# Kernel optimization log

Measured on AMD Instinct MI355X. Metric: run time of the kernel, lower is better.

## Reference

```python
import jax, jax.numpy as jnp
import numpy as np

HIDDEN = 1024
HEADS = 16
BATCH = 2
SEQ = 2048
# dropout_p = 0.1 but module evaluated in eval mode (training=False) -> identity


def setup_inputs() -> dict:
    key = jax.random.key(0)
    k1, k2, k3 = jax.random.split(key, 3)
    x = jax.random.normal(k1, (BATCH, SEQ, HIDDEN), dtype=jnp.float32)
    # unit-scaling Linear: weight ~ N(0,1) (reset_parameters uses nn.init.normal_)
    w_qkv = jax.random.normal(k2, (3 * HIDDEN, HIDDEN), dtype=jnp.float32)
    w_o = jax.random.normal(k3, (HIDDEN, HIDDEN), dtype=jnp.float32)
    return {"x": x, "w_qkv": w_qkv, "w_o": w_o}


def reference(x, w_qkv, w_o):
    b, s, hid = x.shape
    heads = HEADS
    d = hid // heads
    # unit-scaled linear (constraint='to_output_scale'): y = x @ W.T * fan_in**-0.5
    qkv = (x @ w_qkv.T) * (hid ** -0.5)            # [b, s, 3*hid]
    # einops 'b s (z h d) -> z b h s d'
    qkv = qkv.reshape(b, s, 3, heads, d)
    q = jnp.transpose(qkv[:, :, 0], (0, 2, 1, 3))   # [b, h, s, d]
    k = jnp.transpose(qkv[:, :, 1], (0, 2, 1, 3))
    v = jnp.transpose(qkv[:, :, 2], (0, 2, 1, 3))
    # unit-scaled matmul: scale = inner_dim**-0.5
    scores = jnp.einsum('bhqd,bhkd->bhqk', q, k) * (d ** -0.5)  # [b, h, s, s]
    # unit-scaled softmax: output_scale = n / sqrt(n - 1)
    attn = jax.nn.softmax(scores, axis=-1) * (s / np.sqrt(s - 1.0))
    # dropout inactive (eval mode)
    out = jnp.einsum('bhqk,bhkd->bhqd', attn, v) * (s ** -0.5)  # inner dim = s
    out = jnp.transpose(out, (0, 2, 1, 3)).reshape(b, s, hid)   # 'b h s d -> b s (h d)'
    return (out @ w_o.T) * (hid ** -0.5)
```

## Files before the change

### kernel.cpp

```cpp
#include <hip/hip_runtime.h>

typedef unsigned short u16;
typedef _Float16 f16x8 __attribute__((ext_vector_type(8)));
typedef float f32x4 __attribute__((ext_vector_type(4)));
typedef unsigned short u16x4 __attribute__((ext_vector_type(4)));

#define HID 1024
#define SEQ 2048
#define NH 16
#define DH 64

__device__ __forceinline__ u16 f2h(float f) {
  return __builtin_bit_cast(u16, (_Float16)f);
}
__device__ __forceinline__ f32x4 mfma_h(f16x8 a, f16x8 b, f32x4 c) {
  return __builtin_amdgcn_mfma_f32_16x16x32_f16(a, b, c, 0, 0, 0);
}
__device__ __forceinline__ float fexp2(float x) {
#if __has_builtin(__builtin_amdgcn_exp2f)
  return __builtin_amdgcn_exp2f(x);
#else
  return __expf(0.69314718f * x);
#endif
}
__device__ __forceinline__ void g2l16(const u16* g, u16* l) {
  __builtin_amdgcn_global_load_lds(
      (const __attribute__((address_space(1))) unsigned int*)g,
      (__attribute__((address_space(3))) unsigned int*)l, 16, 0, 0);
}

#define NX4 ((4096 * 1024) / 4)
#define NQ4 ((3072 * 1024) / 4)
#define NO4 ((1024 * 1024) / 4)
__global__ __launch_bounds__(256) void prep_kernel(
    const float* __restrict__ x, const float* __restrict__ wq,
    const float* __restrict__ wo,
    u16* __restrict__ x16, u16* __restrict__ wq16, u16* __restrict__ wo16) {
  int i = blockIdx.x * 256 + threadIdx.x;
  const float4 v = (i < NX4) ? ((const float4*)x)[i]
                 : (i < NX4 + NQ4) ? ((const float4*)wq)[i - NX4]
                 : ((const float4*)wo)[i - NX4 - NQ4];
  u16* dst = (i < NX4) ? &x16[(size_t)i * 4]
           : (i < NX4 + NQ4) ? &wq16[(size_t)(i - NX4) * 4]
           : &wo16[(size_t)(i - NX4 - NQ4) * 4];
  u16x4 o;
  o[0] = f2h(v.x); o[1] = f2h(v.y); o[2] = f2h(v.z); o[3] = f2h(v.w);
  *(u16x4*)dst = o;
}

__global__ __launch_bounds__(256, 3) void gemm_qkv(
    const u16* __restrict__ a16, const u16* __restrict__ b16,
    u16* __restrict__ qf, u16* __restrict__ kf, u16* __restrict__ vtf) {
  __shared__ __align__(16) u16 la[128 * 32], lb[128 * 32];
  const int t = threadIdx.x;
  const int lane = t & 63, w = t >> 6;
  const int wr = w >> 1, wc = w & 1;
  const int lr = lane & 15, lg = lane >> 4;
  const int br = blockIdx.x, bc = blockIdx.y;
  const f32x4 fzero = {0.f, 0.f, 0.f, 0.f};
  f32x4 acc[4][4];
#pragma unroll
  for (int i = 0; i < 4; ++i)
#pragma unroll
    for (int j = 0; j < 4; ++j) acc[i][j] = fzero;
  const int srow = t >> 2, scol = (t & 3) << 3;
  const u16* ga = a16 + (size_t)(br * 128 + srow) * HID + scol;
  const u16* gb = b16 + (size_t)(bc * 128 + srow) * HID + scol;
  const int lo16 = t * 8;
  for (int kk = 0; kk < HID; kk += 32) {
    g2l16(ga + kk, &la[lo16]);
    g2l16(ga + kk + (size_t)64 * HID, &la[lo16 + 2048]);
    g2l16(gb + kk, &lb[lo16]);
    g2l16(gb + kk + (size_t)64 * HID, &lb[lo16 + 2048]);
    __syncthreads();
    f16x8 ah[4], bh[4];
#pragma unroll
    for (int i = 0; i < 4; ++i)
      ah[i] = *(const f16x8*)&la[(wr * 64 + i * 16 + lr) * 32 + lg * 8];
#pragma unroll
    for (int j = 0; j < 4; ++j)
      bh[j] = *(const f16x8*)&lb[(wc * 64 + j * 16 + lr) * 32 + lg * 8];
#pragma unroll
    for (int i = 0; i < 4; ++i)
#pragma unroll
      for (int j = 0; j < 4; ++j) acc[i][j] = mfma_h(ah[i], bh[j], acc[i][j]);
    __syncthreads();
  }
  const int m0 = br * 128 + wr * 64, n0 = bc * 128 + wc * 64;
#pragma unroll
  for (int i = 0; i < 4; ++i)
#pragma unroll
    for (int j = 0; j < 4; ++j)
#pragma unroll
      for (int r = 0; r < 4; ++r) {
        int row = m0 + i * 16 + lg * 4 + r;
        int col = n0 + j * 16 + lr;
        float val = acc[i][j][r] * 0.03125f;
        int b = row >> 11, s = row & 2047;
        int z = col >> 10, hh = (col >> 6) & 15, d = col & 63;
        int bhid = b * NH + hh;
        if (z == 0) {
          qf[((size_t)bhid * SEQ + s) * DH + d] = f2h(val * 0.18033688f);
        } else if (z == 1) {
          kf[((size_t)bhid * SEQ + s) * DH + d] = f2h(val);
        } else {
          int s2 = (s & ~63) | ((s & 15) << 2) | ((s >> 4) & 3);
          vtf[((size_t)bhid * DH + d) * SEQ + s2] = f2h(val);
        }
      }
}

__global__ __launch_bounds__(256, 2) void gemm_proj(
    const u16* __restrict__ a16, const u16* __restrict__ b16,
    float* __restrict__ out) {
  __shared__ __align__(16) u16 la[128 * 32];
  __shared__ __align__(16) u16 lb[64 * 32];
  const int t = threadIdx.x;
  const int lane = t & 63, w = t >> 6;
  const int wr = w >> 1, wc = w & 1;
  const int lr = lane & 15, lg = lane >> 4;
  const int br = blockIdx.x, bc = blockIdx.y;
  const f32x4 fzero = {0.f, 0.f, 0.f, 0.f};
  f32x4 acc[4][2];
#pragma unroll
  for (int i = 0; i < 4; ++i)
#pragma unroll
    for (int j = 0; j < 2; ++j) acc[i][j] = fzero;
  const int srow = t >> 2, scol = (t & 3) << 3;
  const u16* ga = a16 + (size_t)(br * 128 + srow) * HID + scol;
  const u16* gb = b16 + (size_t)(bc * 64 + srow) * HID + scol;
  const int lo16 = t * 8;
  for (int kk = 0; kk < HID; kk += 32) {
    g2l16(ga + kk, &la[lo16]);
    g2l16(ga + kk + (size_t)64 * HID, &la[lo16 + 2048]);
    g2l16(gb + kk, &lb[lo16]);
    __syncthreads();
    f16x8 ah[4], bh[2];
#pragma unroll
    for (int i = 0; i < 4; ++i)
      ah[i] = *(const f16x8*)&la[(wr * 64 + i * 16 + lr) * 32 + lg * 8];
#pragma unroll
    for (int j = 0; j < 2; ++j)
      bh[j] = *(const f16x8*)&lb[(wc * 32 + j * 16 + lr) * 32 + lg * 8];
#pragma unroll
    for (int i = 0; i < 4; ++i)
#pragma unroll
      for (int j = 0; j < 2; ++j)
        acc[i][j] = mfma_h(ah[i], bh[j], acc[i][j]);
    __syncthreads();
  }
  const int m0 = br * 128 + wr * 64, n0 = bc * 64 + wc * 32;
#pragma unroll
  for (int i = 0; i < 4; ++i)
#pragma unroll
    for (int j = 0; j < 2; ++j)
#pragma unroll
      for (int r = 0; r < 4; ++r) {
        int row = m0 + i * 16 + lg * 4 + r;
        int col = n0 + j * 16 + lr;
        out[(size_t)row * HID + col] = acc[i][j][r] * 0.03125f;
      }
}

__global__ __launch_bounds__(256, 2) void attn_kernel(
    const u16* __restrict__ qf, const u16* __restrict__ kf,
    const u16* __restrict__ vtf, u16* __restrict__ o16) {
  __shared__ __align__(16) u16 lk[2][64 * 64];
  __shared__ __align__(16) u16 lv[2][64 * 64];
  __shared__ __align__(16) u16 lp[128 * 64];
  const int t = threadIdx.x;
  const int lane = t & 63, w = t >> 6;
  const int lr = lane & 15, lg = lane >> 4;
  const int bh = blockIdx.x, qt = blockIdx.y;
  const size_t base_qk = (size_t)bh * SEQ * DH;
  const size_t base_vt = (size_t)bh * DH * SEQ;

  f16x8 qfr[2][2];
#pragma unroll
  for (int rt = 0; rt < 2; ++rt)
#pragma unroll
    for (int ks = 0; ks < 2; ++ks)
      qfr[rt][ks] = *(const f16x8*)&qf[base_qk +
          (size_t)(qt * 128 + w * 32 + rt * 16 + lr) * DH + ks * 32 + lg * 8];

  const f32x4 fzero = {0.f, 0.f, 0.f, 0.f};
  f32x4 acc_o[2][4];
  float l_i[2][4];
#pragma unroll
  for (int rt = 0; rt < 2; ++rt)
#pragma unroll
    for (int r = 0; r < 4; ++r) l_i[rt][r] = 0.f;
#pragma unroll
  for (int rt = 0; rt < 2; ++rt)
#pragma unroll
    for (int ct = 0; ct < 4; ++ct) acc_o[rt][ct] = fzero;

  const int srow = t >> 3;
  const int scol = ((t & 7) ^ (srow & 7)) << 3;
  const int lo16 = t * 8;

  const u16* gk0 = kf + base_qk + (size_t)srow * DH + scol;
  const u16* gv0 = vtf + base_vt + (size_t)srow * SEQ + scol;

#define STAGE(buf, j)                                             \
  {                                                               \
    const u16* gk = gk0 + (size_t)(j) * 64 * DH;                  \
    g2l16(gk, &lk[buf][lo16]);                                    \
    g2l16(gk + 32 * DH, &lk[buf][lo16 + 2048]);                   \
    const u16* gv = gv0 + (j) * 64;                               \
    g2l16(gv, &lv[buf][lo16]);                                    \
    g2l16(gv + (size_t)32 * SEQ, &lv[buf][lo16 + 2048]);          \
  }

  STAGE(0, 0)

  for (int j = 0; j < SEQ / 64; ++j) {
    const int cur = j & 1;
    __syncthreads();

    f32x4 sa[2][4];
#pragma unroll
    for (int rt = 0; rt < 2; ++rt)
#pragma unroll
      for (int ct = 0; ct < 4; ++ct) sa[rt][ct] = fzero;
#pragma unroll
    for (int ks = 0; ks < 2; ++ks)
#pragma unroll
      for (int ct = 0; ct < 4; ++ct) {
        int row = ct * 16 + lr;
        f16x8 kfr = *(const f16x8*)&lk[cur][row * 64 + (((ks * 4 + lg) ^ (row & 7)) << 3)];
#pragma unroll
        for (int rt = 0; rt < 2; ++rt) sa[rt][ct] = mfma_h(qfr[rt][ks], kfr, sa[rt][ct]);
      }

#pragma unroll
    for (int rt = 0; rt < 2; ++rt)
#pragma unroll
      for (int r = 0; r < 4; ++r) {
        float p0 = fexp2(sa[rt][0][r]);
        float p1 = fexp2(sa[rt][1][r]);
        float p2 = fexp2(sa[rt][2][r]);
        float p3 = fexp2(sa[rt][3][r]);
        l_i[rt][r] += (p0 + p1) + (p2 + p3);
        int prow = w * 32 + rt * 16 + lg * 4 + r;
        u16x4 pk;
        pk[0] = f2h(p0); pk[1] = f2h(p1); pk[2] = f2h(p2); pk[3] = f2h(p3);
        int phys = prow * 64 + ((((lr >> 1) ^ (prow & 7)) << 3) | ((lr & 1) << 2));
        *(u16x4*)&lp[phys] = pk;
      }
    __syncthreads();

    if (j + 1 < SEQ / 64) STAGE(cur ^ 1, j + 1)

#pragma unroll
    for (int ks = 0; ks < 2; ++ks) {
      f16x8 pfr[2];
#pragma unroll
      for (int rt = 0; rt < 2; ++rt) {
        int prow = w * 32 + rt * 16 + lr;
        pfr[rt] = *(const f16x8*)&lp[prow * 64 + (((ks * 4 + lg) ^ (prow & 7)) << 3)];
      }
#pragma unroll
      for (int ct = 0; ct < 4; ++ct) {
        int vrow = ct * 16 + lr;
        f16x8 vfr = *(const f16x8*)&lv[cur][vrow * 64 + (((ks * 4 + lg) ^ (vrow & 7)) << 3)];
#pragma unroll
        for (int rt = 0; rt < 2; ++rt) acc_o[rt][ct] = mfma_h(pfr[rt], vfr, acc_o[rt][ct]);
      }
    }
  }

#pragma unroll
  for (int rt = 0; rt < 2; ++rt)
#pragma unroll
    for (int r = 0; r < 4; ++r) {
      float l = l_i[rt][r];
      l += __shfl_xor(l, 1, 16);
      l += __shfl_xor(l, 2, 16);
      l += __shfl_xor(l, 4, 16);
      l += __shfl_xor(l, 8, 16);
      l_i[rt][r] = l;
    }

  const int b = bh >> 4, hh = bh & 15;
  const float fact = 1.00024426f;
#pragma unroll
  for (int rt = 0; rt < 2; ++rt)
#pragma unroll
    for (int r = 0; r < 4; ++r) {
      float inv = fact / l_i[rt][r];
      int s = qt * 128 + w * 32 + rt * 16 + lg * 4 + r;
#pragma unroll
      for (int ct = 0; ct < 4; ++ct) {
        int d = ct * 16 + lr;
        float val = acc_o[rt][ct][r] * inv;
        o16[((size_t)(b * SEQ + s)) * HID + hh * DH + d] = f2h(val);
      }
    }
}

extern "C" void kernel_launch(void* const* d_in, const int* in_sizes, int n_in,
                              void* d_out, int out_size, void* d_ws, size_t ws_size,
                              hipStream_t stream) {
  const float* x = (const float*)d_in[0];
  const float* w_qkv = (const float*)d_in[1];
  const float* w_o = (const float*)d_in[2];
  u16* ws = (u16*)d_ws;
  const size_t XS = (size_t)4096 * 1024;
  const size_t WQ = (size_t)3072 * 1024;
  const size_t WO = (size_t)1024 * 1024;
  u16* x16  = ws;           u16* wq16 = x16 + XS;
  u16* wo16 = wq16 + WQ;
  u16* q_f  = wo16 + WO;    u16* k_f  = q_f + XS;
  u16* vt_f = k_f + XS;     u16* o16  = vt_f + XS;

  prep_kernel<<<(NX4 + NQ4 + NO4) / 256, 256, 0, stream>>>(
      x, w_qkv, w_o, x16, wq16, wo16);
  gemm_qkv<<<dim3(32, 24), 256, 0, stream>>>(x16, wq16, q_f, k_f, vt_f);
  attn_kernel<<<dim3(32, 16), 256, 0, stream>>>(q_f, k_f, vt_f, o16);
  gemm_proj<<<dim3(32, 16), 256, 0, stream>>>(o16, wo16, (float*)d_out);
}
```

Baseline: 184.9 us.

## Load K fragments directly from global into registers, bypassing LDS

```diff
diff --git a/kernel.cpp b/kernel.cpp
--- a/kernel.cpp
+++ b/kernel.cpp
@@ -165,7 +165,6 @@
 __global__ __launch_bounds__(256, 2) void attn_kernel(
     const u16* __restrict__ qf, const u16* __restrict__ kf,
     const u16* __restrict__ vtf, u16* __restrict__ o16) {
-  __shared__ __align__(16) u16 lk[2][64 * 64];
   __shared__ __align__(16) u16 lv[2][64 * 64];
   __shared__ __align__(16) u16 lp[128 * 64];
   const int t = threadIdx.x;
@@ -195,79 +194,81 @@
 #pragma unroll
     for (int ct = 0; ct < 4; ++ct) acc_o[rt][ct] = fzero;
 
+  const u16* kb = kf + base_qk + (size_t)lr * DH + lg * 8;
+  f16x8 k0[8], k1[8];
+
+#define LOADK(J, KR)                                                      \
+  _Pragma("unroll") for (int ks = 0; ks < 2; ++ks)                        \
+  _Pragma("unroll") for (int ct = 0; ct < 4; ++ct)                        \
+    KR[ks * 4 + ct] =                                                     \
+        *(const f16x8*)&kb[(size_t)((J) * 64 + ct * 16) * DH + ks * 32];
+
   const int srow = t >> 3;
   const int scol = ((t & 7) ^ (srow & 7)) << 3;
   const int lo16 = t * 8;
-
-  const u16* gk0 = kf + base_qk + (size_t)srow * DH + scol;
   const u16* gv0 = vtf + base_vt + (size_t)srow * SEQ + scol;
 
 #define STAGE(buf, j)                                             \
   {                                                               \
-    const u16* gk = gk0 + (size_t)(j) * 64 * DH;                  \
-    g2l16(gk, &lk[buf][lo16]);                                    \
-    g2l16(gk + 32 * DH, &lk[buf][lo16 + 2048]);                   \
     const u16* gv = gv0 + (j) * 64;                               \
     g2l16(gv, &lv[buf][lo16]);                                    \
     g2l16(gv + (size_t)32 * SEQ, &lv[buf][lo16 + 2048]);          \
   }
 
+#define ATTN_ITER(J, KC, KN)                                              \
+  {                                                                       \
+    const int cur = (J) & 1;                                              \
+    __syncthreads();               \
+    f32x4 sa[2][4];                                                       \
+    _Pragma("unroll") for (int rt = 0; rt < 2; ++rt)                      \
+    _Pragma("unroll") for (int ct = 0; ct < 4; ++ct) sa[rt][ct] = fzero;  \
+    _Pragma("unroll") for (int ks = 0; ks < 2; ++ks)                      \
+    _Pragma("unroll") for (int ct = 0; ct < 4; ++ct) {                    \
+      _Pragma("unroll") for (int rt = 0; rt < 2; ++rt)                    \
+        sa[rt][ct] = mfma_h(qfr[rt][ks], KC[ks * 4 + ct], sa[rt][ct]);    \
+    }                                                                     \
+    _Pragma("unroll") for (int rt = 0; rt < 2; ++rt)                      \
+    _Pragma("unroll") for (int r = 0; r < 4; ++r) {                       \
+      float p0 = fexp2(sa[rt][0][r]);                                     \
+      float p1 = fexp2(sa[rt][1][r]);                                     \
+      float p2 = fexp2(sa[rt][2][r]);                                     \
+      float p3 = fexp2(sa[rt][3][r]);                                     \
+      l_i[rt][r] += (p0 + p1) + (p2 + p3);                                \
+      int prow = w * 32 + rt * 16 + lg * 4 + r;                           \
+      u16x4 pk;                                                           \
+      pk[0] = f2h(p0); pk[1] = f2h(p1); pk[2] = f2h(p2); pk[3] = f2h(p3); \
+      int phys = prow * 64 +                                              \
+                 ((((lr >> 1) ^ (prow & 7)) << 3) | ((lr & 1) << 2));     \
+      *(u16x4*)&lp[phys] = pk;                                            \
+    }                                                                     \
+    __syncthreads();                                      \
+    if ((J) + 1 < SEQ / 64) {                                             \
+      LOADK((J) + 1, KN)                 \
+      STAGE(((J) + 1) & 1, (J) + 1)                                       \
+    }                                                                     \
+    _Pragma("unroll") for (int ks = 0; ks < 2; ++ks) {                    \
+      f16x8 pfr[2];                                                       \
+      _Pragma("unroll") for (int rt = 0; rt < 2; ++rt) {                  \
+        int prow = w * 32 + rt * 16 + lr;                                 \
+        pfr[rt] = *(const f16x8*)&lp[prow * 64 +                          \
+                    (((ks * 4 + lg) ^ (prow & 7)) << 3)];                 \
+      }                                                                   \
+      _Pragma("unroll") for (int ct = 0; ct < 4; ++ct) {                  \
+        int vrow = ct * 16 + lr;                                          \
+        f16x8 vfr = *(const f16x8*)&lv[cur][vrow * 64 +                   \
+                    (((ks * 4 + lg) ^ (vrow & 7)) << 3)];                 \
+        _Pragma("unroll") for (int rt = 0; rt < 2; ++rt)                  \
+          acc_o[rt][ct] = mfma_h(pfr[rt], vfr, acc_o[rt][ct]);            \
+      }                                                                   \
+    }                                                                     \
+  }
+
+  LOADK(0, k0)
   STAGE(0, 0)
 
-  for (int j = 0; j < SEQ / 64; ++j) {
-    const int cur = j & 1;
-    __syncthreads();
-
-    f32x4 sa[2][4];
-#pragma unroll
-    for (int rt = 0; rt < 2; ++rt)
-#pragma unroll
-      for (int ct = 0; ct < 4; ++ct) sa[rt][ct] = fzero;
-#pragma unroll
-    for (int ks = 0; ks < 2; ++ks)
-#pragma unroll
-      for (int ct = 0; ct < 4; ++ct) {
-        int row = ct * 16 + lr;
-        f16x8 kfr = *(const f16x8*)&lk[cur][row * 64 + (((ks * 4 + lg) ^ (row & 7)) << 3)];
-#pragma unroll
-        for (int rt = 0; rt < 2; ++rt) sa[rt][ct] = mfma_h(qfr[rt][ks], kfr, sa[rt][ct]);
-      }
-
-#pragma unroll
-    for (int rt = 0; rt < 2; ++rt)
-#pragma unroll
-      for (int r = 0; r < 4; ++r) {
-        float p0 = fexp2(sa[rt][0][r]);
-        float p1 = fexp2(sa[rt][1][r]);
-        float p2 = fexp2(sa[rt][2][r]);
-        float p3 = fexp2(sa[rt][3][r]);
-        l_i[rt][r] += (p0 + p1) + (p2 + p3);
-        int prow = w * 32 + rt * 16 + lg * 4 + r;
-        u16x4 pk;
-        pk[0] = f2h(p0); pk[1] = f2h(p1); pk[2] = f2h(p2); pk[3] = f2h(p3);
-        int phys = prow * 64 + ((((lr >> 1) ^ (prow & 7)) << 3) | ((lr & 1) << 2));
-        *(u16x4*)&lp[phys] = pk;
-      }
-    __syncthreads();
-
-    if (j + 1 < SEQ / 64) STAGE(cur ^ 1, j + 1)
-
-#pragma unroll
-    for (int ks = 0; ks < 2; ++ks) {
-      f16x8 pfr[2];
-#pragma unroll
-      for (int rt = 0; rt < 2; ++rt) {
-        int prow = w * 32 + rt * 16 + lr;
-        pfr[rt] = *(const f16x8*)&lp[prow * 64 + (((ks * 4 + lg) ^ (prow & 7)) << 3)];
-      }
-#pragma unroll
-      for (int ct = 0; ct < 4; ++ct) {
-        int vrow = ct * 16 + lr;
-        f16x8 vfr = *(const f16x8*)&lv[cur][vrow * 64 + (((ks * 4 + lg) ^ (vrow & 7)) << 3)];
-#pragma unroll
-        for (int rt = 0; rt < 2; ++rt) acc_o[rt][ct] = mfma_h(pfr[rt], vfr, acc_o[rt][ct]);
-      }
-    }
+  for (int j = 0; j < SEQ / 64; j += 2) {
+    ATTN_ITER(j, k0, k1)
+    ATTN_ITER(j + 1, k1, k0)
   }
 
 #pragma unroll
```

Result: slower. 211.2 us (+14.3%).

## Transpose softmax probabilities in registers via identity MFMA instead of LDS

Applied to the files above, without the earlier changes.

```diff
diff --git a/kernel.cpp b/kernel.cpp
--- a/kernel.cpp
+++ b/kernel.cpp
@@ -2,6 +2,7 @@
 
 typedef unsigned short u16;
 typedef _Float16 f16x8 __attribute__((ext_vector_type(8)));
+typedef _Float16 f16x4 __attribute__((ext_vector_type(4)));
 typedef float f32x4 __attribute__((ext_vector_type(4)));
 typedef unsigned short u16x4 __attribute__((ext_vector_type(4)));
 
@@ -15,6 +16,9 @@
 }
 __device__ __forceinline__ f32x4 mfma_h(f16x8 a, f16x8 b, f32x4 c) {
   return __builtin_amdgcn_mfma_f32_16x16x32_f16(a, b, c, 0, 0, 0);
+}
+__device__ __forceinline__ f32x4 mfma_h16(f16x4 a, f16x4 b, f32x4 c) {
+  return __builtin_amdgcn_mfma_f32_16x16x16f16(a, b, c, 0, 0, 0);
 }
 __device__ __forceinline__ float fexp2(float x) {
 #if __has_builtin(__builtin_amdgcn_exp2f)
@@ -104,7 +108,10 @@
         } else if (z == 1) {
           kf[((size_t)bhid * SEQ + s) * DH + d] = f2h(val);
         } else {
-          int s2 = (s & ~63) | ((s & 15) << 2) | ((s >> 4) & 3);
+          int kv = s & 63;
+          int ct = kv >> 4, lgv = (kv >> 2) & 3, rv = kv & 3;
+          int kvp = ((ct >> 1) << 5) | (lgv << 3) | ((ct & 1) << 2) | rv;
+          int s2 = (s & ~63) | kvp;
           vtf[((size_t)bhid * DH + d) * SEQ + s2] = f2h(val);
         }
       }
@@ -167,7 +174,6 @@
     const u16* __restrict__ vtf, u16* __restrict__ o16) {
   __shared__ __align__(16) u16 lk[2][64 * 64];
   __shared__ __align__(16) u16 lv[2][64 * 64];
-  __shared__ __align__(16) u16 lp[128 * 64];
   const int t = threadIdx.x;
   const int lane = t & 63, w = t >> 6;
   const int lr = lane & 15, lg = lane >> 4;
@@ -182,6 +188,10 @@
     for (int ks = 0; ks < 2; ++ks)
       qfr[rt][ks] = *(const f16x8*)&qf[base_qk +
           (size_t)(qt * 128 + w * 32 + rt * 16 + lr) * DH + ks * 32 + lg * 8];
+
+  f16x4 bI;
+#pragma unroll
+  for (int j = 0; j < 4; ++j) bI[j] = (_Float16)((lr == lg * 4 + j) ? 1.0f : 0.0f);
 
   const f32x4 fzero = {0.f, 0.f, 0.f, 0.f};
   f32x4 acc_o[2][4];
@@ -233,41 +243,42 @@
         for (int rt = 0; rt < 2; ++rt) sa[rt][ct] = mfma_h(qfr[rt][ks], kfr, sa[rt][ct]);
       }
 
-#pragma unroll
-    for (int rt = 0; rt < 2; ++rt)
-#pragma unroll
-      for (int r = 0; r < 4; ++r) {
-        float p0 = fexp2(sa[rt][0][r]);
-        float p1 = fexp2(sa[rt][1][r]);
-        float p2 = fexp2(sa[rt][2][r]);
-        float p3 = fexp2(sa[rt][3][r]);
-        l_i[rt][r] += (p0 + p1) + (p2 + p3);
-        int prow = w * 32 + rt * 16 + lg * 4 + r;
-        u16x4 pk;
-        pk[0] = f2h(p0); pk[1] = f2h(p1); pk[2] = f2h(p2); pk[3] = f2h(p3);
-        int phys = prow * 64 + ((((lr >> 1) ^ (prow & 7)) << 3) | ((lr & 1) << 2));
-        *(u16x4*)&lp[phys] = pk;
-      }
-    __syncthreads();
-
     if (j + 1 < SEQ / 64) STAGE(cur ^ 1, j + 1)
 
-#pragma unroll
-    for (int ks = 0; ks < 2; ++ks) {
-      f16x8 pfr[2];
-#pragma unroll
-      for (int rt = 0; rt < 2; ++rt) {
-        int prow = w * 32 + rt * 16 + lr;
-        pfr[rt] = *(const f16x8*)&lp[prow * 64 + (((ks * 4 + lg) ^ (prow & 7)) << 3)];
-      }
+    f16x8 pfr[2][2];
+#pragma unroll
+    for (int rt = 0; rt < 2; ++rt) {
+      f32x4 tr[4];
+#pragma unroll
+      for (int ct = 0; ct < 4; ++ct) {
+        f16x4 a4;
+#pragma unroll
+        for (int r = 0; r < 4; ++r) {
+          float p = fexp2(sa[rt][ct][r]);
+          l_i[rt][r] += p;
+          a4[r] = (_Float16)p;
+        }
+        tr[ct] = mfma_h16(a4, bI, fzero);
+      }
+#pragma unroll
+      for (int ks = 0; ks < 2; ++ks) {
+        f16x8 pf;
+#pragma unroll
+        for (int j2 = 0; j2 < 8; ++j2)
+          pf[j2] = (_Float16)tr[ks * 2 + (j2 >> 2)][j2 & 3];
+        pfr[rt][ks] = pf;
+      }
+    }
+
+#pragma unroll
+    for (int ks = 0; ks < 2; ++ks)
 #pragma unroll
       for (int ct = 0; ct < 4; ++ct) {
         int vrow = ct * 16 + lr;
         f16x8 vfr = *(const f16x8*)&lv[cur][vrow * 64 + (((ks * 4 + lg) ^ (vrow & 7)) << 3)];
 #pragma unroll
-        for (int rt = 0; rt < 2; ++rt) acc_o[rt][ct] = mfma_h(pfr[rt], vfr, acc_o[rt][ct]);
-      }
-    }
+        for (int rt = 0; rt < 2; ++rt) acc_o[rt][ct] = mfma_h(pfr[rt][ks], vfr, acc_o[rt][ct]);
+      }
   }
 
 #pragma unroll
```

New measurement: 176.8 us. 4.3% less time.
